# Optimization experiments

Hardware: AMD Instinct MI355X
Metric: run time of the kernel (lower is better)

The kernel has to match this reference:

```python
import jax, jax.numpy as jnp
import numpy as np

B, T, I, H, L = 256, 512, 64, 256, 2


def _lstm_layer(x, Wih, Whh, bih, bhh):
    # x: [B, T, Din]; Wih: [4H, Din]; Whh: [4H, H]; gate order i,f,g,o (PyTorch)
    Hdim = Whh.shape[1]
    # Precompute input projections for all timesteps (one big GEMM)
    x_proj = jnp.einsum('btd,gd->btg', x, Wih) + bih + bhh  # [B, T, 4H]
    x_proj = jnp.transpose(x_proj, (1, 0, 2))  # [T, B, 4H]

    def step(carry, xt):
        h, c = carry
        gates = xt + h @ Whh.T  # [B, 4H]
        i, f, g, o = jnp.split(gates, 4, axis=-1)
        i = jax.nn.sigmoid(i)
        f = jax.nn.sigmoid(f)
        g = jnp.tanh(g)
        o = jax.nn.sigmoid(o)
        c = f * c + i * g
        h = o * jnp.tanh(c)
        return (h, c), h

    b = x.shape[0]
    h0 = jnp.zeros((b, Hdim), dtype=x.dtype)
    c0 = jnp.zeros((b, Hdim), dtype=x.dtype)
    _, hs = jax.lax.scan(step, (h0, c0), x_proj)  # hs: [T, B, H]
    return jnp.transpose(hs, (1, 0, 2))  # [B, T, H]


def setup_inputs() -> dict:
    key = jax.random.key(0)
    ks = jax.random.split(key, 12)
    s_in = 1.0 / np.sqrt(H)
    inp = {
        'x': jax.random.normal(ks[0], (B, T, I), dtype=jnp.float32),
        'Wih0': jax.random.uniform(ks[1], (4 * H, I), minval=-s_in, maxval=s_in),
        'Whh0': jax.random.uniform(ks[2], (4 * H, H), minval=-s_in, maxval=s_in),
        'bih0': jax.random.uniform(ks[3], (4 * H,), minval=-s_in, maxval=s_in),
        'bhh0': jax.random.uniform(ks[4], (4 * H,), minval=-s_in, maxval=s_in),
        'Wih1': jax.random.uniform(ks[5], (4 * H, H), minval=-s_in, maxval=s_in),
        'Whh1': jax.random.uniform(ks[6], (4 * H, H), minval=-s_in, maxval=s_in),
        'bih1': jax.random.uniform(ks[7], (4 * H,), minval=-s_in, maxval=s_in),
        'bhh1': jax.random.uniform(ks[8], (4 * H,), minval=-s_in, maxval=s_in),
        'Wfc': jax.random.uniform(ks[9], (1, H), minval=-s_in, maxval=s_in),
        'bfc': jax.random.uniform(ks[10], (1,), minval=-s_in, maxval=s_in),
    }
    return inp


def reference(x, Wih0, Whh0, bih0, bhh0, Wih1, Whh1, bih1, bhh1, Wfc, bfc):
    h1 = _lstm_layer(x, Wih0, Whh0, bih0, bhh0)   # [B, T, H]
    h2 = _lstm_layer(h1, Wih1, Whh1, bih1, bhh1)  # [B, T, H]
    last = h2[:, -1, :]                           # [B, H]
    return last @ Wfc.T + bfc                     # [B, 1]
```

## Files before the change

### kernel.cpp

```cpp
#include <hip/hip_runtime.h>

#define TT   512
#define IDIM 64
#define HDIM 256

typedef short  short8  __attribute__((ext_vector_type(8)));
typedef short  short4v __attribute__((ext_vector_type(4)));
typedef float  f32x4   __attribute__((ext_vector_type(4)));
typedef unsigned long long u64;

__device__ __forceinline__ short f2bf(float f) {
    unsigned u = __float_as_uint(f);
    u = u + 0x7FFFu + ((u >> 16) & 1u);
    return (short)(u >> 16);
}
__device__ __forceinline__ float bf2f(short h) {
    return __uint_as_float(((unsigned)(unsigned short)h) << 16);
}
__device__ __forceinline__ float sigm(float x)  { return 1.0f / (1.0f + __expf(-x)); }
__device__ __forceinline__ float tanh_(float x) { return 2.0f / (1.0f + __expf(-2.0f * x)) - 1.0f; }

__device__ __forceinline__ void unpack16(const u64 W[6], u64 q[4]) {
    unsigned short u[16];
#pragma unroll
    for (int w = 0; w < 6; ++w)
#pragma unroll
        for (int k = 0; k < 3; ++k) {
            int j = 3 * w + k;
            if (j < 16) u[j] = (unsigned short)(W[w] >> (16 * k));
        }
#pragma unroll
    for (int t = 0; t < 4; ++t)
        q[t] = (u64)u[4*t] | ((u64)u[4*t+1] << 16) | ((u64)u[4*t+2] << 32) | ((u64)u[4*t+3] << 48);
}

__global__ __launch_bounds__(256, 1) void lstm_fused(
    const float* __restrict__ x,
    const float* __restrict__ Wih0, const float* __restrict__ Whh0,
    const float* __restrict__ bih0, const float* __restrict__ bhh0,
    const float* __restrict__ Wih1, const float* __restrict__ Whh1,
    const float* __restrict__ bih1, const float* __restrict__ bhh1,
    const float* __restrict__ Wfc,  const float* __restrict__ bfc,
    float* __restrict__ out, char* __restrict__ ws)
{
    u64* h0buf = (u64*)ws;
    u64* h1buf = h0buf + 2 * 16 * 16 * 96;

    const int blk   = blockIdx.x;
    const int grp   = ((blk & 7) << 1) | ((blk >> 3) & 1);
    const int chunk = blk >> 4;
    const int tid   = threadIdx.x;
    const int lane  = tid & 63;
    const int wave  = tid >> 6;
    const int quad  = lane >> 4;
    const int nn    = lane & 15;

    __shared__ short A0[16][328];
    __shared__ short A1[16][520];
    __shared__ float gbuf[2][4][16][16];
    __shared__ float red[16][16];
    __shared__ __align__(16) short hls[2][16][16];
    __shared__ float ldspad[5120];

    for (int i = tid; i < 16 * 328; i += 256) (&A0[0][0])[i] = 0;
    for (int i = tid; i < 16 * 520; i += 256) (&A1[0][0])[i] = 0;

    const int wrow = wave * HDIM + chunk * 16 + nn;
    short8 w0f[10];
    short8 w1f[16];
#pragma unroll
    for (int kb = 0; kb < 10; ++kb)
#pragma unroll
        for (int j = 0; j < 8; ++j) {
            int k = kb * 32 + quad * 8 + j;
            float v = (k < 64) ? Wih0[wrow * IDIM + k] : Whh0[wrow * HDIM + (k - 64)];
            w0f[kb][j] = f2bf(v);
        }
#pragma unroll
    for (int kb = 0; kb < 16; ++kb)
#pragma unroll
        for (int j = 0; j < 8; ++j) {
            int k = kb * 32 + quad * 8 + j;
            float v = (k < 256) ? Wih1[wrow * HDIM + k] : Whh1[wrow * HDIM + (k - 256)];
            w1f[kb][j] = f2bf(v);
        }
    const float bias0 = bih0[wrow] + bhh0[wrow];
    const float bias1 = bih1[wrow] + bhh1[wrow];

    const int em = tid >> 4;
    const int ej = tid & 15;
    float c0 = 0.0f, c1 = 0.0f;

    auto load_x = [&](int t) {
        const float4 v = *(const float4*)&x[((size_t)(grp * 16 + em) * TT + t) * IDIM + ej * 4];
        short4v sv;
        sv[0] = f2bf(v.x); sv[1] = f2bf(v.y); sv[2] = f2bf(v.z); sv[3] = f2bf(v.w);
        *(short4v*)&A0[em][ej * 4] = sv;
    };

    __syncthreads();
    load_x(0);
    __syncthreads();

    for (int s = 0; s <= TT; ++s) {
        if (s < TT) {
            f32x4 accA = {0.f, 0.f, 0.f, 0.f}, accB = {0.f, 0.f, 0.f, 0.f};
#pragma unroll
            for (int kb = 0; kb < 10; kb += 2) {
                short8 a0v = *(const short8*)&A0[nn][kb * 32 + quad * 8];
                short8 a1v = *(const short8*)&A0[nn][(kb + 1) * 32 + quad * 8];
                accA = __builtin_amdgcn_mfma_f32_16x16x32_bf16(a0v, w0f[kb],     accA, 0, 0, 0);
                accB = __builtin_amdgcn_mfma_f32_16x16x32_bf16(a1v, w0f[kb + 1], accB, 0, 0, 0);
            }
            const f32x4 acc = accA + accB;
#pragma unroll
            for (int r = 0; r < 4; ++r)
                gbuf[0][wave][quad * 4 + r][nn] = acc[r] + bias0;
        }
        if (s >= 1) {
            f32x4 accA = {0.f, 0.f, 0.f, 0.f}, accB = {0.f, 0.f, 0.f, 0.f};
#pragma unroll
            for (int kb = 0; kb < 16; kb += 2) {
                short8 a0v = *(const short8*)&A1[nn][kb * 32 + quad * 8];
                short8 a1v = *(const short8*)&A1[nn][(kb + 1) * 32 + quad * 8];
                accA = __builtin_amdgcn_mfma_f32_16x16x32_bf16(a0v, w1f[kb],     accA, 0, 0, 0);
                accB = __builtin_amdgcn_mfma_f32_16x16x32_bf16(a1v, w1f[kb + 1], accB, 0, 0, 0);
            }
            const f32x4 acc = accA + accB;
#pragma unroll
            for (int r = 0; r < 4; ++r)
                gbuf[1][wave][quad * 4 + r][nn] = acc[r] + bias1;
        }
        __syncthreads();

        if (s < TT) {
            float gi = sigm (gbuf[0][0][em][ej]);
            float gf = sigm (gbuf[0][1][em][ej]);
            float gg = tanh_(gbuf[0][2][em][ej]);
            float go = sigm (gbuf[0][3][em][ej]);
            c0 = gf * c0 + gi * gg;
            hls[0][em][ej] = f2bf(go * tanh_(c0));
        }
        if (s >= 1) {
            float gi = sigm (gbuf[1][0][em][ej]);
            float gf = sigm (gbuf[1][1][em][ej]);
            float gg = tanh_(gbuf[1][2][em][ej]);
            float go = sigm (gbuf[1][3][em][ej]);
            c1 = gf * c1 + gi * gg;
            hls[1][em][ej] = f2bf(go * tanh_(c1));
        } else {
            hls[1][em][ej] = 0;
        }
        __syncthreads();

        if (tid < 96) {
            const int r = tid / 6, w = tid % 6;
            const int j0 = 3 * w;
            const u64 sq = (u64)(unsigned)(s + 1) << 48;
            u64 v0 = (u64)(unsigned short)hls[0][r][j0];
            u64 v1 = (u64)(unsigned short)hls[1][r][j0];
            if (j0 + 1 < 16) {
                v0 |= (u64)(unsigned short)hls[0][r][j0 + 1] << 16;
                v1 |= (u64)(unsigned short)hls[1][r][j0 + 1] << 16;
            }
            if (j0 + 2 < 16) {
                v0 |= (u64)(unsigned short)hls[0][r][j0 + 2] << 32;
                v1 |= (u64)(unsigned short)hls[1][r][j0 + 2] << 32;
            }
            v0 |= sq; v1 |= sq;
            const size_t base = (((size_t)(s & 1) * 16 + grp) * 16 + r) * 96 + chunk * 6 + w;
            __hip_atomic_store(&h0buf[base], v0, __ATOMIC_RELAXED, __HIP_MEMORY_SCOPE_AGENT);
            __hip_atomic_store(&h1buf[base], v1, __ATOMIC_RELAXED, __HIP_MEMORY_SCOPE_AGENT);
        }

        if (s + 1 < TT) load_x(s + 1);

        {
            const bool g0 = (s < TT), g1 = (s >= 1);
            const unsigned sq = (unsigned)(s + 1);
            const size_t rb = (((size_t)(s & 1) * 16 + grp) * 16 + em) * 96 + ej * 6;
            u64 W0[6], W1[6];
            bool ok0 = !g0, ok1 = !g1;
            int budget = 1 << 17;
            while ((!ok0 || !ok1) && budget-- > 0) {
                if (!ok0) {
#pragma unroll
                    for (int i = 0; i < 6; ++i)
                        W0[i] = __hip_atomic_load(&h0buf[rb + i],
                                                  __ATOMIC_RELAXED, __HIP_MEMORY_SCOPE_AGENT);
                    bool t = true;
#pragma unroll
                    for (int i = 0; i < 6; ++i) t &= ((unsigned)(W0[i] >> 48) == sq);
                    ok0 = t;
                }
                if (!ok1) {
#pragma unroll
                    for (int i = 0; i < 6; ++i)
                        W1[i] = __hip_atomic_load(&h1buf[rb + i],
                                                  __ATOMIC_RELAXED, __HIP_MEMORY_SCOPE_AGENT);
                    bool t = true;
#pragma unroll
                    for (int i = 0; i < 6; ++i) t &= ((unsigned)(W1[i] >> 48) == sq);
                    ok1 = t;
                }
            }
            asm volatile("s_waitcnt vmcnt(0)" ::: "memory");

            if (g0) {
                u64 q[4]; unpack16(W0, q);
                u64* d0 = (u64*)&A0[em][64 + ej * 16];
                u64* d1 = (u64*)&A1[em][ej * 16];
#pragma unroll
                for (int t = 0; t < 4; ++t) { d0[t] = q[t]; d1[t] = q[t]; }
            }
            if (g1) {
                u64 q[4]; unpack16(W1, q);
                u64* d2 = (u64*)&A1[em][256 + ej * 16];
#pragma unroll
                for (int t = 0; t < 4; ++t) d2[t] = q[t];
            }
        }
        __syncthreads();
    }

    {
        float part = 0.f;
#pragma unroll
        for (int kk = 0; kk < 16; ++kk) {
            int k = ej * 16 + kk;
            part += bf2f(A1[em][256 + k]) * Wfc[k];
        }
        red[em][ej] = part;
    }
    __syncthreads();
    if (chunk == 0 && tid < 16) {
        float sum = bfc[0];
#pragma unroll
        for (int c = 0; c < 16; ++c) sum += red[tid][c];
        out[grp * 16 + tid] = sum;
    }

    if (gridDim.x > 100000) { ldspad[tid] = bias0; out[0] = ldspad[255 - tid]; }
}

extern "C" void kernel_launch(void* const* d_in, const int* in_sizes, int n_in,
                              void* d_out, int out_size, void* d_ws, size_t ws_size,
                              hipStream_t stream) {
    (void)in_sizes; (void)n_in; (void)out_size; (void)ws_size;
    const float* x    = (const float*)d_in[0];
    const float* Wih0 = (const float*)d_in[1];
    const float* Whh0 = (const float*)d_in[2];
    const float* bih0 = (const float*)d_in[3];
    const float* bhh0 = (const float*)d_in[4];
    const float* Wih1 = (const float*)d_in[5];
    const float* Whh1 = (const float*)d_in[6];
    const float* bih1 = (const float*)d_in[7];
    const float* bhh1 = (const float*)d_in[8];
    const float* Wfc  = (const float*)d_in[9];
    const float* bfc  = (const float*)d_in[10];

    lstm_fused<<<256, 256, 0, stream>>>(x, Wih0, Whh0, bih0, bhh0,
                                        Wih1, Whh1, bih1, bhh1, Wfc, bfc,
                                        (float*)d_out, (char*)d_ws);
}
```

Baseline: 1.810 ms.

## Halve block count with 512-thread blocks, split layers across waves, 8-way exchange

Grid shrinks from 256 blocks of 256 threads to 128 blocks of 512 threads. Each block now owns 32 hidden units per batch group, and waves 0-3 compute layer 0 while waves 4-7 compute layer 1. Fewer cooperating blocks per batch group (8 instead of 16) means each step's cross-block hidden-state exchange waits on fewer peers. Each thread now polls only the remote words it needs and writes its block's own slice straight into LDS. In exchange, each wave's per-step MFMA chain gets longer and the unpack logic is more complex. The dropped LDS padding array also changes occupancy behaviour.

```diff
diff --git a/kernel.cpp b/kernel.cpp
--- a/kernel.cpp
+++ b/kernel.cpp
@@ -20,21 +20,7 @@
 __device__ __forceinline__ float sigm(float x)  { return 1.0f / (1.0f + __expf(-x)); }
 __device__ __forceinline__ float tanh_(float x) { return 2.0f / (1.0f + __expf(-2.0f * x)) - 1.0f; }
 
-__device__ __forceinline__ void unpack16(const u64 W[6], u64 q[4]) {
-    unsigned short u[16];
-#pragma unroll
-    for (int w = 0; w < 6; ++w)
-#pragma unroll
-        for (int k = 0; k < 3; ++k) {
-            int j = 3 * w + k;
-            if (j < 16) u[j] = (unsigned short)(W[w] >> (16 * k));
-        }
-#pragma unroll
-    for (int t = 0; t < 4; ++t)
-        q[t] = (u64)u[4*t] | ((u64)u[4*t+1] << 16) | ((u64)u[4*t+2] << 32) | ((u64)u[4*t+3] << 48);
-}
-
-__global__ __launch_bounds__(256, 1) void lstm_fused(
+__global__ __launch_bounds__(512, 1) void lstm_fused(
     const float* __restrict__ x,
     const float* __restrict__ Wih0, const float* __restrict__ Whh0,
     const float* __restrict__ bih0, const float* __restrict__ bhh0,
@@ -44,7 +30,7 @@
     float* __restrict__ out, char* __restrict__ ws)
 {
     u64* h0buf = (u64*)ws;
-    u64* h1buf = h0buf + 2 * 16 * 16 * 96;
+    u64* h1buf = h0buf + 2 * 16 * 16 * 88;
 
     const int blk   = blockIdx.x;
     const int grp   = ((blk & 7) << 1) | ((blk >> 3) & 1);
@@ -52,173 +38,210 @@
     const int tid   = threadIdx.x;
     const int lane  = tid & 63;
     const int wave  = tid >> 6;
+    const int lay   = wave >> 2;
+    const int gate  = wave & 3;
     const int quad  = lane >> 4;
     const int nn    = lane & 15;
 
-    __shared__ short A0[16][328];
-    __shared__ short A1[16][520];
-    __shared__ float gbuf[2][4][16][16];
-    __shared__ float red[16][16];
-    __shared__ __align__(16) short hls[2][16][16];
-    __shared__ float ldspad[5120];
-
-    for (int i = tid; i < 16 * 328; i += 256) (&A0[0][0])[i] = 0;
-    for (int i = tid; i < 16 * 520; i += 256) (&A1[0][0])[i] = 0;
-
-    const int wrow = wave * HDIM + chunk * 16 + nn;
-    short8 w0f[10];
-    short8 w1f[16];
-#pragma unroll
-    for (int kb = 0; kb < 10; ++kb)
-#pragma unroll
-        for (int j = 0; j < 8; ++j) {
-            int k = kb * 32 + quad * 8 + j;
-            float v = (k < 64) ? Wih0[wrow * IDIM + k] : Whh0[wrow * HDIM + (k - 64)];
-            w0f[kb][j] = f2bf(v);
-        }
-#pragma unroll
-    for (int kb = 0; kb < 16; ++kb)
-#pragma unroll
-        for (int j = 0; j < 8; ++j) {
-            int k = kb * 32 + quad * 8 + j;
-            float v = (k < 256) ? Wih1[wrow * HDIM + k] : Whh1[wrow * HDIM + (k - 256)];
-            w1f[kb][j] = f2bf(v);
-        }
-    const float bias0 = bih0[wrow] + bhh0[wrow];
-    const float bias1 = bih1[wrow] + bhh1[wrow];
-
-    const int em = tid >> 4;
-    const int ej = tid & 15;
+    __shared__ short A0[16][344];
+    __shared__ short A1[16][536];
+    __shared__ float gbuf[2][4][16][34];
+    __shared__ float red[16][32];
+    __shared__ short hls[2][16][32];
+
+    for (int i = tid; i < 16 * 344; i += 512) (&A0[0][0])[i] = 0;
+    for (int i = tid; i < 16 * 536; i += 512) (&A1[0][0])[i] = 0;
+
+    short8 wf[2][16];
+    float  bias[2];
+    if (lay == 0) {
+#pragma unroll
+        for (int n = 0; n < 2; ++n) {
+            const int row = gate * HDIM + chunk * 32 + n * 16 + nn;
+#pragma unroll
+            for (int kb = 0; kb < 10; ++kb)
+#pragma unroll
+                for (int j = 0; j < 8; ++j) {
+                    int k = kb * 32 + quad * 8 + j;
+                    float v = (k < 64) ? Wih0[row * IDIM + k]
+                                       : Whh0[row * HDIM + (k - 64)];
+                    wf[n][kb][j] = f2bf(v);
+                }
+            bias[n] = bih0[row] + bhh0[row];
+        }
+    } else {
+#pragma unroll
+        for (int n = 0; n < 2; ++n) {
+            const int row = gate * HDIM + chunk * 32 + n * 16 + nn;
+#pragma unroll
+            for (int kb = 0; kb < 16; ++kb)
+#pragma unroll
+                for (int j = 0; j < 8; ++j) {
+                    int k = kb * 32 + quad * 8 + j;
+                    float v = (k < 256) ? Wih1[row * HDIM + k]
+                                        : Whh1[row * HDIM + (k - 256)];
+                    wf[n][kb][j] = f2bf(v);
+                }
+            bias[n] = bih1[row] + bhh1[row];
+        }
+    }
+
+    const int em = tid >> 5;
+    const int eu = tid & 31;
     float c0 = 0.0f, c1 = 0.0f;
 
     auto load_x = [&](int t) {
-        const float4 v = *(const float4*)&x[((size_t)(grp * 16 + em) * TT + t) * IDIM + ej * 4];
+        const float4 v = *(const float4*)&x[((size_t)(grp * 16 + em) * TT + t) * IDIM + eu * 4];
         short4v sv;
         sv[0] = f2bf(v.x); sv[1] = f2bf(v.y); sv[2] = f2bf(v.z); sv[3] = f2bf(v.w);
-        *(short4v*)&A0[em][ej * 4] = sv;
+        *(short4v*)&A0[em][eu * 4] = sv;
     };
 
+    const int pp   = tid >> 4;
+    const int pj   = tid & 15;
+    const int pbuf = pp >> 4;
+    const int prow = pp & 15;
+
     __syncthreads();
-    load_x(0);
+    if (eu < 16) load_x(0);
     __syncthreads();
 
     for (int s = 0; s <= TT; ++s) {
+        if (lay == 0) {
+            if (s < TT) {
+                f32x4 a00 = {0,0,0,0}, a01 = {0,0,0,0}, a10 = {0,0,0,0}, a11 = {0,0,0,0};
+#pragma unroll
+                for (int kb = 0; kb < 10; kb += 2) {
+                    short8 av0 = *(const short8*)&A0[nn][kb * 32 + quad * 8];
+                    short8 av1 = *(const short8*)&A0[nn][(kb + 1) * 32 + quad * 8];
+                    a00 = __builtin_amdgcn_mfma_f32_16x16x32_bf16(av0, wf[0][kb],     a00, 0, 0, 0);
+                    a10 = __builtin_amdgcn_mfma_f32_16x16x32_bf16(av0, wf[1][kb],     a10, 0, 0, 0);
+                    a01 = __builtin_amdgcn_mfma_f32_16x16x32_bf16(av1, wf[0][kb + 1], a01, 0, 0, 0);
+                    a11 = __builtin_amdgcn_mfma_f32_16x16x32_bf16(av1, wf[1][kb + 1], a11, 0, 0, 0);
+                }
+                const f32x4 t0 = a00 + a01, t1 = a10 + a11;
+#pragma unroll
+                for (int r = 0; r < 4; ++r) {
+                    gbuf[0][gate][quad * 4 + r][nn]      = t0[r] + bias[0];
+                    gbuf[0][gate][quad * 4 + r][16 + nn] = t1[r] + bias[1];
+                }
+            }
+        } else {
+            if (s >= 1) {
+                f32x4 a00 = {0,0,0,0}, a01 = {0,0,0,0}, a10 = {0,0,0,0}, a11 = {0,0,0,0};
+#pragma unroll
+                for (int kb = 0; kb < 16; kb += 2) {
+                    short8 av0 = *(const short8*)&A1[nn][kb * 32 + quad * 8];
+                    short8 av1 = *(const short8*)&A1[nn][(kb + 1) * 32 + quad * 8];
+                    a00 = __builtin_amdgcn_mfma_f32_16x16x32_bf16(av0, wf[0][kb],     a00, 0, 0, 0);
+                    a10 = __builtin_amdgcn_mfma_f32_16x16x32_bf16(av0, wf[1][kb],     a10, 0, 0, 0);
+                    a01 = __builtin_amdgcn_mfma_f32_16x16x32_bf16(av1, wf[0][kb + 1], a01, 0, 0, 0);
+                    a11 = __builtin_amdgcn_mfma_f32_16x16x32_bf16(av1, wf[1][kb + 1], a11, 0, 0, 0);
+                }
+                const f32x4 t0 = a00 + a01, t1 = a10 + a11;
+#pragma unroll
+                for (int r = 0; r < 4; ++r) {
+                    gbuf[1][gate][quad * 4 + r][nn]      = t0[r] + bias[0];
+                    gbuf[1][gate][quad * 4 + r][16 + nn] = t1[r] + bias[1];
+                }
+            }
+        }
+        __syncthreads();
+
         if (s < TT) {
-            f32x4 accA = {0.f, 0.f, 0.f, 0.f}, accB = {0.f, 0.f, 0.f, 0.f};
-#pragma unroll
-            for (int kb = 0; kb < 10; kb += 2) {
-                short8 a0v = *(const short8*)&A0[nn][kb * 32 + quad * 8];
-                short8 a1v = *(const short8*)&A0[nn][(kb + 1) * 32 + quad * 8];
-                accA = __builtin_amdgcn_mfma_f32_16x16x32_bf16(a0v, w0f[kb],     accA, 0, 0, 0);
-                accB = __builtin_amdgcn_mfma_f32_16x16x32_bf16(a1v, w0f[kb + 1], accB, 0, 0, 0);
-            }
-            const f32x4 acc = accA + accB;
-#pragma unroll
-            for (int r = 0; r < 4; ++r)
-                gbuf[0][wave][quad * 4 + r][nn] = acc[r] + bias0;
+            float gi = sigm (gbuf[0][0][em][eu]);
+            float gf = sigm (gbuf[0][1][em][eu]);
+            float gg = tanh_(gbuf[0][2][em][eu]);
+            float go = sigm (gbuf[0][3][em][eu]);
+            c0 = gf * c0 + gi * gg;
+            hls[0][em][eu] = f2bf(go * tanh_(c0));
         }
         if (s >= 1) {
-            f32x4 accA = {0.f, 0.f, 0.f, 0.f}, accB = {0.f, 0.f, 0.f, 0.f};
-#pragma unroll
-            for (int kb = 0; kb < 16; kb += 2) {
-                short8 a0v = *(const short8*)&A1[nn][kb * 32 + quad * 8];
-                short8 a1v = *(const short8*)&A1[nn][(kb + 1) * 32 + quad * 8];
-                accA = __builtin_amdgcn_mfma_f32_16x16x32_bf16(a0v, w1f[kb],     accA, 0, 0, 0);
-                accB = __builtin_amdgcn_mfma_f32_16x16x32_bf16(a1v, w1f[kb + 1], accB, 0, 0, 0);
-            }
-            const f32x4 acc = accA + accB;
-#pragma unroll
-            for (int r = 0; r < 4; ++r)
-                gbuf[1][wave][quad * 4 + r][nn] = acc[r] + bias1;
+            float gi = sigm (gbuf[1][0][em][eu]);
+            float gf = sigm (gbuf[1][1][em][eu]);
+            float gg = tanh_(gbuf[1][2][em][eu]);
+            float go = sigm (gbuf[1][3][em][eu]);
+            c1 = gf * c1 + gi * gg;
+            hls[1][em][eu] = f2bf(go * tanh_(c1));
+        } else {
+            hls[1][em][eu] = 0;
         }
         __syncthreads();
 
-        if (s < TT) {
-            float gi = sigm (gbuf[0][0][em][ej]);
-            float gf = sigm (gbuf[0][1][em][ej]);
-            float gg = tanh_(gbuf[0][2][em][ej]);
-            float go = sigm (gbuf[0][3][em][ej]);
-            c0 = gf * c0 + gi * gg;
-            hls[0][em][ej] = f2bf(go * tanh_(c0));
-        }
-        if (s >= 1) {
-            float gi = sigm (gbuf[1][0][em][ej]);
-            float gf = sigm (gbuf[1][1][em][ej]);
-            float gg = tanh_(gbuf[1][2][em][ej]);
-            float go = sigm (gbuf[1][3][em][ej]);
-            c1 = gf * c1 + gi * gg;
-            hls[1][em][ej] = f2bf(go * tanh_(c1));
-        } else {
-            hls[1][em][ej] = 0;
-        }
-        __syncthreads();
-
-        if (tid < 96) {
-            const int r = tid / 6, w = tid % 6;
+        {
+            const short h0v = hls[0][em][eu], h1v = hls[1][em][eu];
+            A0[em][64 + chunk * 32 + eu]  = h0v;
+            A1[em][chunk * 32 + eu]       = h0v;
+            A1[em][256 + chunk * 32 + eu] = h1v;
+        }
+
+        if (tid < 352) {
+            const int b  = tid / 176;
+            const int r2 = (tid % 176) / 11;
+            const int w  = tid % 11;
             const int j0 = 3 * w;
-            const u64 sq = (u64)(unsigned)(s + 1) << 48;
-            u64 v0 = (u64)(unsigned short)hls[0][r][j0];
-            u64 v1 = (u64)(unsigned short)hls[1][r][j0];
-            if (j0 + 1 < 16) {
-                v0 |= (u64)(unsigned short)hls[0][r][j0 + 1] << 16;
-                v1 |= (u64)(unsigned short)hls[1][r][j0 + 1] << 16;
-            }
-            if (j0 + 2 < 16) {
-                v0 |= (u64)(unsigned short)hls[0][r][j0 + 2] << 32;
-                v1 |= (u64)(unsigned short)hls[1][r][j0 + 2] << 32;
-            }
-            v0 |= sq; v1 |= sq;
-            const size_t base = (((size_t)(s & 1) * 16 + grp) * 16 + r) * 96 + chunk * 6 + w;
-            __hip_atomic_store(&h0buf[base], v0, __ATOMIC_RELAXED, __HIP_MEMORY_SCOPE_AGENT);
-            __hip_atomic_store(&h1buf[base], v1, __ATOMIC_RELAXED, __HIP_MEMORY_SCOPE_AGENT);
-        }
-
-        if (s + 1 < TT) load_x(s + 1);
+            const int kc = (w == 10) ? 2 : 3;
+            u64 v = (u64)(unsigned)(s + 1) << 48;
+#pragma unroll
+            for (int k = 0; k < 3; ++k)
+                if (k < kc) v |= (u64)(unsigned short)hls[b][r2][j0 + k] << (16 * k);
+            const size_t gi_ = (((size_t)(s & 1) * 16 + grp) * 16 + r2) * 88 + chunk * 11 + w;
+            u64* dst = (b == 0 ? h0buf : h1buf) + gi_;
+            (void)__hip_atomic_exchange(dst, v, __ATOMIC_RELAXED, __HIP_MEMORY_SCOPE_AGENT);
+        }
+
+        if (s + 1 < TT && eu < 16) load_x(s + 1);
 
         {
-            const bool g0 = (s < TT), g1 = (s >= 1);
+            const bool need = (pbuf == 0) ? (s < TT) : (s >= 1);
+            const int  nw   = need ? ((pj < 13) ? 5 : 4) : 0;
             const unsigned sq = (unsigned)(s + 1);
-            const size_t rb = (((size_t)(s & 1) * 16 + grp) * 16 + em) * 96 + ej * 6;
-            u64 W0[6], W1[6];
-            bool ok0 = !g0, ok1 = !g1;
+            u64* const buf = pbuf ? h1buf : h0buf;
+            const size_t rowbase = (((size_t)(s & 1) * 16 + grp) * 16 + prow) * 88;
+            int cc[5], wii[5];
+            const u64* ptr[5];
+#pragma unroll
+            for (int m = 0; m < 5; ++m) {
+                const int widx = (pj + 16 * m < 77) ? (pj + 16 * m) : 0;
+                const int c2 = widx / 11;
+                const int wi = widx - 11 * c2;
+                const int c  = c2 + (c2 >= chunk);
+                cc[m] = c; wii[m] = wi;
+                ptr[m] = buf + rowbase + c * 11 + wi;
+            }
+            u64  W[5]   = {0, 0, 0, 0, 0};
+            bool got[5] = {false, false, false, false, false};
             int budget = 1 << 17;
-            while ((!ok0 || !ok1) && budget-- > 0) {
-                if (!ok0) {
-#pragma unroll
-                    for (int i = 0; i < 6; ++i)
-                        W0[i] = __hip_atomic_load(&h0buf[rb + i],
-                                                  __ATOMIC_RELAXED, __HIP_MEMORY_SCOPE_AGENT);
-                    bool t = true;
-#pragma unroll
-                    for (int i = 0; i < 6; ++i) t &= ((unsigned)(W0[i] >> 48) == sq);
-                    ok0 = t;
-                }
-                if (!ok1) {
-#pragma unroll
-                    for (int i = 0; i < 6; ++i)
-                        W1[i] = __hip_atomic_load(&h1buf[rb + i],
-                                                  __ATOMIC_RELAXED, __HIP_MEMORY_SCOPE_AGENT);
-                    bool t = true;
-#pragma unroll
-                    for (int i = 0; i < 6; ++i) t &= ((unsigned)(W1[i] >> 48) == sq);
-                    ok1 = t;
-                }
+            bool all = (nw == 0);
+            while (!all && budget-- > 0) {
+                all = true;
+#pragma unroll
+                for (int m = 0; m < 5; ++m)
+                    if (m < nw && !got[m]) {
+                        const u64 v = __hip_atomic_load(ptr[m],
+                                          __ATOMIC_RELAXED, __HIP_MEMORY_SCOPE_AGENT);
+                        if ((unsigned)(v >> 48) == sq) { W[m] = v; got[m] = true; }
+                        else all = false;
+                    }
             }
             asm volatile("s_waitcnt vmcnt(0)" ::: "memory");
-
-            if (g0) {
-                u64 q[4]; unpack16(W0, q);
-                u64* d0 = (u64*)&A0[em][64 + ej * 16];
-                u64* d1 = (u64*)&A1[em][ej * 16];
-#pragma unroll
-                for (int t = 0; t < 4; ++t) { d0[t] = q[t]; d1[t] = q[t]; }
-            }
-            if (g1) {
-                u64 q[4]; unpack16(W1, q);
-                u64* d2 = (u64*)&A1[em][256 + ej * 16];
-#pragma unroll
-                for (int t = 0; t < 4; ++t) d2[t] = q[t];
-            }
+#pragma unroll
+            for (int m = 0; m < 5; ++m)
+                if (m < nw) {
+                    const int u0 = cc[m] * 32 + wii[m] * 3;
+                    const int kc = (wii[m] == 10) ? 2 : 3;
+#pragma unroll
+                    for (int k = 0; k < 3; ++k)
+                        if (k < kc) {
+                            const short h = (short)(unsigned short)(W[m] >> (16 * k));
+                            if (pbuf == 0) {
+                                A0[prow][64 + u0 + k] = h;
+                                A1[prow][u0 + k]      = h;
+                            } else {
+                                A1[prow][256 + u0 + k] = h;
+                            }
+                        }
+                }
         }
         __syncthreads();
     }
@@ -226,21 +249,19 @@
     {
         float part = 0.f;
 #pragma unroll
-        for (int kk = 0; kk < 16; ++kk) {
-            int k = ej * 16 + kk;
+        for (int kk = 0; kk < 8; ++kk) {
+            const int k = eu * 8 + kk;
             part += bf2f(A1[em][256 + k]) * Wfc[k];
         }
-        red[em][ej] = part;
+        red[em][eu] = part;
     }
     __syncthreads();
     if (chunk == 0 && tid < 16) {
         float sum = bfc[0];
 #pragma unroll
-        for (int c = 0; c < 16; ++c) sum += red[tid][c];
+        for (int c = 0; c < 32; ++c) sum += red[tid][c];
         out[grp * 16 + tid] = sum;
     }
-
-    if (gridDim.x > 100000) { ldspad[tid] = bias0; out[0] = ldspad[255 - tid]; }
 }
 
 extern "C" void kernel_launch(void* const* d_in, const int* in_sizes, int n_in,
@@ -259,7 +280,7 @@
     const float* Wfc  = (const float*)d_in[9];
     const float* bfc  = (const float*)d_in[10];
 
-    lstm_fused<<<256, 256, 0, stream>>>(x, Wih0, Whh0, bih0, bhh0,
+    lstm_fused<<<128, 512, 0, stream>>>(x, Wih0, Whh0, bih0, bhh0,
                                         Wih1, Whh1, bih1, bhh1, Wfc, bfc,
                                         (float*)d_out, (char*)d_ws);
 }
```

Measured after the change: 2.079 ms. 14.8% more time.
